# Optimization experiments

Measured on AMD Instinct MI355X. Metric: run time of the kernel, lower is better.

Reference implementation:

```python
import jax, jax.numpy as jnp
import numpy as np

N_NODES = 100000
N_EDGES = 1000000
D_FEAT = 128
N_ACTIONS = 64


def setup_inputs() -> dict:
    key = jax.random.key(0)
    ks = jax.random.split(key, 8)
    return {
        "x": jax.random.normal(ks[0], (N_NODES, D_FEAT), dtype=jnp.float32),
        "edge_index": jax.random.randint(ks[1], (2, N_EDGES), 0, N_NODES, dtype=jnp.int64),
        "W_gcn": jax.random.normal(ks[2], (D_FEAT, D_FEAT), dtype=jnp.float32) / np.sqrt(D_FEAT),
        "b_gcn": jax.random.normal(ks[3], (D_FEAT,), dtype=jnp.float32) * 0.02,
        "W_high": jax.random.normal(ks[4], (D_FEAT, N_ACTIONS), dtype=jnp.float32) / np.sqrt(D_FEAT),
        "b_high": jax.random.normal(ks[5], (N_ACTIONS,), dtype=jnp.float32) * 0.02,
        "W_low": jax.random.normal(ks[6], (D_FEAT, N_ACTIONS), dtype=jnp.float32) / np.sqrt(D_FEAT),
        "b_low": jax.random.normal(ks[7], (N_ACTIONS,), dtype=jnp.float32) * 0.02,
    }


def gcn_conv(x, edge_index, W, b):
    """PyG GCNConv: add self-loops, symmetric normalization, aggregate, linear."""
    n = x.shape[0]
    loops = jnp.arange(n, dtype=edge_index.dtype)
    src = jnp.concatenate([edge_index[0], loops])  # message sources
    dst = jnp.concatenate([edge_index[1], loops])  # message targets
    # degree of each target node (edge weight 1, incl. self-loop)
    deg = jax.ops.segment_sum(jnp.ones(src.shape[0], dtype=x.dtype), dst, num_segments=n)
    dinv = jax.lax.rsqrt(deg)  # deg >= 1 thanks to self-loops
    norm = dinv[src] * dinv[dst]  # [E+N]
    h = x @ W  # [N, D] dense transform first (cheaper than transforming messages)
    agg = jax.ops.segment_sum(h[src] * norm[:, None], dst, num_segments=n)
    return agg + b


def reference(x, edge_index, W_gcn, b_gcn, W_high, b_high, W_low, b_low):
    h = gcn_conv(x, edge_index, W_gcn, b_gcn)  # [N, D]
    high = h @ W_high + b_high  # [N, A]
    low = h @ W_low + b_low     # [N, A]
    return (high, low)
```

## Files before the change

### kernel.cpp

```cpp
#include <hip/hip_runtime.h>


#define BLOCK 256
#define SB 512
#define NB_MAX 784
#define CONV_BLOCKS 4096

typedef _Float16 half8 __attribute__((ext_vector_type(8)));
typedef _Float16 half2v __attribute__((ext_vector_type(2)));
typedef float f32x4 __attribute__((ext_vector_type(4)));

__device__ inline unsigned short f2bf(float f) {
    unsigned u = __float_as_uint(f);
    unsigned r = (u + 0x7FFF + ((u >> 16) & 1)) >> 16;
    return (unsigned short)r;
}
__device__ inline float bf2f(unsigned short u) {
    return __uint_as_float(((unsigned)u) << 16);
}


__global__ __launch_bounds__(BLOCK) void k_prep(const float* __restrict__ x,
                                                const int* __restrict__ dst, int E,
                                                const float* __restrict__ Wg,
                                                const float* __restrict__ Wh,
                                                const float* __restrict__ Wl,
                                                const float* __restrict__ bg,
                                                const float* __restrict__ bh,
                                                const float* __restrict__ bl,
                                                _Float16* __restrict__ WfT,
                                                float* __restrict__ bf,
                                                int* __restrict__ hist_g,
                                                unsigned short* __restrict__ xh,
                                                int n, int NB) {
    __shared__ int hist[NB_MAX];
    int b = blockIdx.x;
    if (b < 16) {
        int r = b * 8 + (threadIdx.x >> 5);
        int c0 = (threadIdx.x & 31) * 4;
        float a0 = 0.f, a1 = 0.f, a2 = 0.f, a3 = 0.f;
        for (int j = 0; j < 128; j++) {
            float wg = Wg[r * 128 + j];
            float4 wc;
            if (c0 < 64) wc = *(const float4*)(Wh + j * 64 + c0);
            else         wc = *(const float4*)(Wl + j * 64 + (c0 - 64));
            a0 += wg * wc.x; a1 += wg * wc.y; a2 += wg * wc.z; a3 += wg * wc.w;
        }
        WfT[(size_t)(c0 + 0) * 128 + r] = (_Float16)a0;
        WfT[(size_t)(c0 + 1) * 128 + r] = (_Float16)a1;
        WfT[(size_t)(c0 + 2) * 128 + r] = (_Float16)a2;
        WfT[(size_t)(c0 + 3) * 128 + r] = (_Float16)a3;
    } else if (b == 16) {
        int c = threadIdx.x;
        if (c < 128) {
            float acc = (c < 64) ? bh[c] : bl[c - 64];
            for (int j = 0; j < 128; j++) {
                float wc = (c < 64) ? Wh[j * 64 + c] : Wl[j * 64 + (c - 64)];
                acc += bg[j] * wc;
            }
            bf[c] = acc;
        }
    } else if (b < 17 + SB) {
        int blk = b - 17;
        for (int i = threadIdx.x; i < NB; i += BLOCK) hist[i] = 0;
        __syncthreads();
        int chunk = (E + SB - 1) / SB;
        int e0 = blk * chunk, e1 = min(E, e0 + chunk);
        for (int e = e0 + threadIdx.x; e < e1; e += BLOCK)
            atomicAdd(&hist[dst[e] >> 7], 1);
        __syncthreads();
        for (int i = threadIdx.x; i < NB; i += BLOCK)
            hist_g[(size_t)i * SB + blk] = hist[i];
    } else {
        const float4* x4 = (const float4*)x;
        ushort4* o4 = (ushort4*)xh;
        int total = n * 32;
        int i = (b - 17 - SB) * BLOCK + threadIdx.x;
        int stride = CONV_BLOCKS * BLOCK;
        for (; i < total; i += stride) {
            float4 v = x4[i];
            ushort4 o;
            o.x = f2bf(v.x); o.y = f2bf(v.y); o.z = f2bf(v.z); o.w = f2bf(v.w);
            o4[i] = o;
        }
    }
}


__global__ __launch_bounds__(BLOCK) void k_scanA(int* __restrict__ hist_g,
                                                 int* __restrict__ bucketTotal, int NB) {
    __shared__ int s[SB];
    int bkt = blockIdx.x;
    int t = threadIdx.x;
    int a0 = hist_g[(size_t)bkt * SB + t];
    int a1 = hist_g[(size_t)bkt * SB + t + 256];
    s[t] = a0; s[t + 256] = a1;
    __syncthreads();
    for (int ofs = 1; ofs < SB; ofs <<= 1) {
        int v0 = (t >= ofs) ? s[t - ofs] : 0;
        int v1 = (t + 256 >= ofs) ? s[t + 256 - ofs] : 0;
        __syncthreads();
        s[t] += v0; s[t + 256] += v1;
        __syncthreads();
    }
    hist_g[(size_t)bkt * SB + t] = s[t] - a0;
    hist_g[(size_t)bkt * SB + t + 256] = s[t + 256] - a1;
    if (t == 255) bucketTotal[bkt] = s[SB - 1];
}


__global__ __launch_bounds__(1024) void k_scanB(const int* __restrict__ bucketTotal,
                                                int* __restrict__ bucketStart,
                                                int NB, int E) {
    __shared__ int s[1024];
    int t = threadIdx.x;
    int v = (t < NB) ? bucketTotal[t] : 0;
    s[t] = v;
    __syncthreads();
    for (int ofs = 1; ofs < 1024; ofs <<= 1) {
        int u = (t >= ofs) ? s[t - ofs] : 0;
        __syncthreads();
        s[t] += u;
        __syncthreads();
    }
    if (t < NB) bucketStart[t] = s[t] - v;
    if (t == NB - 1) bucketStart[NB] = E;
}


__global__ __launch_bounds__(BLOCK) void k_scatter(const int* __restrict__ src,
                                                   const int* __restrict__ dst, int E,
                                                   const int* __restrict__ hist_g,
                                                   const int* __restrict__ bucketStart,
                                                   int2* __restrict__ ebuf, int NB) {
    __shared__ int cur[NB_MAX];
    int blk = blockIdx.x;
    for (int i = threadIdx.x; i < NB; i += BLOCK)
        cur[i] = bucketStart[i] + hist_g[(size_t)i * SB + blk];
    __syncthreads();
    int chunk = (E + SB - 1) / SB;
    int e0 = blk * chunk, e1 = min(E, e0 + chunk);
    for (int e = e0 + threadIdx.x; e < e1; e += BLOCK) {
        int d = dst[e];
        int pos = atomicAdd(&cur[d >> 7], 1);
        ebuf[pos] = make_int2(d, src[e]);
    }
}


__global__ __launch_bounds__(BLOCK) void k_node(const int2* __restrict__ ebuf,
                                                const int* __restrict__ bucketStart,
                                                int* __restrict__ off,
                                                float* __restrict__ dinv,
                                                int* __restrict__ csr,
                                                int n, int NB, int E) {
    __shared__ int cnt[128];
    __shared__ int pre[128];
    __shared__ int cur[128];
    int bkt = blockIdx.x;
    int t = threadIdx.x;
    int node0 = bkt << 7;
    int nn = min(128, n - node0);
    int eb0 = bucketStart[bkt], eb1 = bucketStart[bkt + 1];

    if (t < 128) cnt[t] = 0;
    __syncthreads();
    for (int e = eb0 + t; e < eb1; e += BLOCK)
        atomicAdd(&cnt[ebuf[e].x & 127], 1);
    __syncthreads();
    if (t < 128) pre[t] = cnt[t];
    __syncthreads();
    for (int ofs = 1; ofs < 128; ofs <<= 1) {
        int v = (t < 128 && t >= ofs) ? pre[t - ofs] : 0;
        __syncthreads();
        if (t < 128) pre[t] += v;
        __syncthreads();
    }
    if (t < 128) cur[t] = pre[t] - cnt[t];
    __syncthreads();
    if (t < nn) {
        off[node0 + t] = eb0 + cur[t];
        dinv[node0 + t] = rsqrtf((float)(cnt[t] + 1));
    }
    if (bkt == 0 && t == 0) off[n] = E;
    for (int e = eb0 + t; e < eb1; e += BLOCK) {
        int2 p = ebuf[e];
        int pos = atomicAdd(&cur[p.x & 127], 1);
        csr[eb0 + pos] = p.y;
    }
}


__global__ __launch_bounds__(BLOCK) void k_gather(const int* __restrict__ off,
                                                  const int* __restrict__ csr,
                                                  const float* __restrict__ dinv,
                                                  const unsigned short* __restrict__ xh,
                                                  const float* __restrict__ x,
                                                  _Float16* __restrict__ aggh, int n) {
    int wave = (blockIdx.x * blockDim.x + threadIdx.x) >> 6;
    int lane = threadIdx.x & 63;
    if (wave >= n) return;
    int d = wave;
    int beg = off[d], end = off[d + 1];

    float accx = 0.f, accy = 0.f;
    for (int base = beg; base < end; base += 64) {
        int cnt = min(64, end - base);
        int s = 0; float w = 0.f;
        if (lane < cnt) { s = csr[base + lane]; w = dinv[s]; }
        int j = 0;
        for (; j + 4 <= cnt; j += 4) {
            int s0 = __shfl(s, j);
            int s1 = __shfl(s, j + 1);
            int s2 = __shfl(s, j + 2);
            int s3 = __shfl(s, j + 3);
            float w0 = __shfl(w, j);
            float w1 = __shfl(w, j + 1);
            float w2 = __shfl(w, j + 2);
            float w3 = __shfl(w, j + 3);
            ushort2 v0 = ((const ushort2*)(xh + (size_t)s0 * 128))[lane];
            ushort2 v1 = ((const ushort2*)(xh + (size_t)s1 * 128))[lane];
            ushort2 v2 = ((const ushort2*)(xh + (size_t)s2 * 128))[lane];
            ushort2 v3 = ((const ushort2*)(xh + (size_t)s3 * 128))[lane];
            accx += w0 * bf2f(v0.x) + w1 * bf2f(v1.x) + w2 * bf2f(v2.x) + w3 * bf2f(v3.x);
            accy += w0 * bf2f(v0.y) + w1 * bf2f(v1.y) + w2 * bf2f(v2.y) + w3 * bf2f(v3.y);
        }
        for (; j < cnt; j++) {
            int sj = __shfl(s, j);
            float wj = __shfl(w, j);
            ushort2 v = ((const ushort2*)(xh + (size_t)sj * 128))[lane];
            accx += wj * bf2f(v.x);
            accy += wj * bf2f(v.y);
        }
    }
    float dv = dinv[d];
    float2 xv = ((const float2*)(x + (size_t)d * 128))[lane];
    half2v o;
    o.x = (_Float16)(dv * accx + dv * dv * xv.x);
    o.y = (_Float16)(dv * accy + dv * dv * xv.y);
    ((half2v*)(aggh + (size_t)d * 128))[lane] = o;
}


__global__ __launch_bounds__(BLOCK) void k_final(const _Float16* __restrict__ aggh,
                                                 const _Float16* __restrict__ WfT,
                                                 const float* __restrict__ bf,
                                                 float* __restrict__ out, int n) {
    int wave = threadIdx.x >> 6;
    int lane = threadIdx.x & 63;
    int l15 = lane & 15;
    int lk = lane >> 4;
    int row_base = blockIdx.x * 128 + wave * 32;

    half8 a[2][4];
#pragma unroll
    for (int rf = 0; rf < 2; rf++) {
        int r = row_base + rf * 16 + l15;
        if (r >= n) r = n - 1;
        const _Float16* ap = aggh + (size_t)r * 128 + lk * 8;
#pragma unroll
        for (int kk = 0; kk < 4; kk++)
            a[rf][kk] = *(const half8*)(ap + kk * 32);
    }

    f32x4 acc[2][8];
#pragma unroll
    for (int rf = 0; rf < 2; rf++)
#pragma unroll
        for (int cf = 0; cf < 8; cf++)
            acc[rf][cf] = (f32x4){0.f, 0.f, 0.f, 0.f};

#pragma unroll
    for (int kk = 0; kk < 4; kk++) {
#pragma unroll
        for (int cf = 0; cf < 8; cf++) {
            const _Float16* bp = WfT + (size_t)(cf * 16 + l15) * 128 + kk * 32 + lk * 8;
            half8 bfr = *(const half8*)bp;
#pragma unroll
            for (int rf = 0; rf < 2; rf++)
                acc[rf][cf] = __builtin_amdgcn_mfma_f32_16x16x32_f16(
                    a[rf][kk], bfr, acc[rf][cf], 0, 0, 0);
        }
    }

#pragma unroll
    for (int cf = 0; cf < 8; cf++) {
        int c = cf * 16 + l15;
        float bv = bf[c];
        size_t cbase = (c < 64) ? (size_t)c : (size_t)n * 64 + (size_t)(c - 64);
#pragma unroll
        for (int rf = 0; rf < 2; rf++) {
            int r0 = row_base + rf * 16 + lk * 4;
#pragma unroll
            for (int j = 0; j < 4; j++) {
                int r = r0 + j;
                if (r < n) out[cbase + (size_t)r * 64] = acc[rf][cf][j] + bv;
            }
        }
    }
}

extern "C" void kernel_launch(void* const* d_in, const int* in_sizes, int n_in,
                              void* d_out, int out_size, void* d_ws, size_t ws_size,
                              hipStream_t stream) {
    const float* x  = (const float*)d_in[0];
    const int*   ei = (const int*)d_in[1];
    const float* Wg = (const float*)d_in[2];
    const float* bg = (const float*)d_in[3];
    const float* Wh = (const float*)d_in[4];
    const float* bh = (const float*)d_in[5];
    const float* Wl = (const float*)d_in[6];
    const float* bl = (const float*)d_in[7];
    float* out = (float*)d_out;

    int n = in_sizes[0] / 128;
    int E = in_sizes[1] / 2;
    const int* src = ei;
    const int* dst = ei + E;
    int NB = (n + 127) >> 7;

    char* ws = (char*)d_ws;
    int*   hist_g      = (int*)ws;                ws += (size_t)NB_MAX * SB * 4;
    int*   bucketTotal = (int*)ws;                ws += (size_t)NB_MAX * 4;
    int*   bucketStart = (int*)ws;                ws += (size_t)(NB_MAX + 2) * 4;
    int2*  ebuf        = (int2*)ws;               ws += (size_t)E * 8;
    int*   off         = (int*)ws;                ws += (size_t)(n + 1) * 4;
    float* dinv        = (float*)ws;              ws += (size_t)n * 4;
    int*   csr         = (int*)ws;                ws += (size_t)E * 4;
    _Float16* aggh     = (_Float16*)ws;           ws += (size_t)n * 128 * 2;
    _Float16* WfT      = (_Float16*)ws;           ws += (size_t)128 * 128 * 2;
    float* bf          = (float*)ws;              ws += (size_t)128 * 4;
    unsigned short* xh = (unsigned short*)ws;

    k_prep<<<17 + SB + CONV_BLOCKS, BLOCK, 0, stream>>>(
        x, dst, E, Wg, Wh, Wl, bg, bh, bl, WfT, bf, hist_g, xh, n, NB);
    k_scanA<<<NB, BLOCK, 0, stream>>>(hist_g, bucketTotal, NB);
    k_scanB<<<1, 1024, 0, stream>>>(bucketTotal, bucketStart, NB, E);
    k_scatter<<<SB, BLOCK, 0, stream>>>(src, dst, E, hist_g, bucketStart, ebuf, NB);
    k_node<<<NB, BLOCK, 0, stream>>>(ebuf, bucketStart, off, dinv, csr, n, NB, E);
    k_gather<<<((size_t)n * 64 + BLOCK - 1) / BLOCK, BLOCK, 0, stream>>>(
        off, csr, dinv, xh, x, aggh, n);
    k_final<<<(n + 127) / 128, BLOCK, 0, stream>>>(aggh, WfT, bf, out, n);
}
```

Measured before the change: 273.2 us.

## Gather with 16-byte half8 loads, four edges per wave step, fp16 features

The gather kernel now splits each wave into four 16-lane groups. Each group processes a different edge and each lane loads 16 bytes (8 fp16 values), where before the whole wave walked one edge with 4-byte loads. Partial sums are combined across groups with xor shuffles, and the self-loop term now reads the fp16 copy instead of the fp32 input. The staged features switch from bf16 to fp16, and workspace buffers get 256-byte alignment. The wider loads and more edges in flight are meant to raise memory-level parallelism. The cost is extra reduction shuffles, wasted lanes when an edge chunk is not a multiple of four (handled via zero weights), and fp16 range and precision tradeoffs.

```diff
diff --git a/kernel.cpp b/kernel.cpp
--- a/kernel.cpp
+++ b/kernel.cpp
@@ -7,17 +7,8 @@
 #define CONV_BLOCKS 4096
 
 typedef _Float16 half8 __attribute__((ext_vector_type(8)));
-typedef _Float16 half2v __attribute__((ext_vector_type(2)));
+typedef _Float16 half4 __attribute__((ext_vector_type(4)));
 typedef float f32x4 __attribute__((ext_vector_type(4)));
-
-__device__ inline unsigned short f2bf(float f) {
-    unsigned u = __float_as_uint(f);
-    unsigned r = (u + 0x7FFF + ((u >> 16) & 1)) >> 16;
-    return (unsigned short)r;
-}
-__device__ inline float bf2f(unsigned short u) {
-    return __uint_as_float(((unsigned)u) << 16);
-}
 
 
 __global__ __launch_bounds__(BLOCK) void k_prep(const float* __restrict__ x,
@@ -31,7 +22,7 @@
                                                 _Float16* __restrict__ WfT,
                                                 float* __restrict__ bf,
                                                 int* __restrict__ hist_g,
-                                                unsigned short* __restrict__ xh,
+                                                _Float16* __restrict__ xh,
                                                 int n, int NB) {
     __shared__ int hist[NB_MAX];
     int b = blockIdx.x;
@@ -73,14 +64,15 @@
             hist_g[(size_t)i * SB + blk] = hist[i];
     } else {
         const float4* x4 = (const float4*)x;
-        ushort4* o4 = (ushort4*)xh;
+        half4* o4 = (half4*)xh;
         int total = n * 32;
         int i = (b - 17 - SB) * BLOCK + threadIdx.x;
         int stride = CONV_BLOCKS * BLOCK;
         for (; i < total; i += stride) {
             float4 v = x4[i];
-            ushort4 o;
-            o.x = f2bf(v.x); o.y = f2bf(v.y); o.z = f2bf(v.z); o.w = f2bf(v.w);
+            half4 o;
+            o.x = (_Float16)v.x; o.y = (_Float16)v.y;
+            o.z = (_Float16)v.z; o.w = (_Float16)v.w;
             o4[i] = o;
         }
     }
@@ -194,51 +186,49 @@
 __global__ __launch_bounds__(BLOCK) void k_gather(const int* __restrict__ off,
                                                   const int* __restrict__ csr,
                                                   const float* __restrict__ dinv,
-                                                  const unsigned short* __restrict__ xh,
-                                                  const float* __restrict__ x,
+                                                  const _Float16* __restrict__ xh,
                                                   _Float16* __restrict__ aggh, int n) {
     int wave = (blockIdx.x * blockDim.x + threadIdx.x) >> 6;
     int lane = threadIdx.x & 63;
     if (wave >= n) return;
     int d = wave;
     int beg = off[d], end = off[d + 1];
-
-    float accx = 0.f, accy = 0.f;
+    int g = lane >> 4;
+    int sl = lane & 15;
+
+    float acc[8];
+#pragma unroll
+    for (int k = 0; k < 8; k++) acc[k] = 0.f;
+
     for (int base = beg; base < end; base += 64) {
         int cnt = min(64, end - base);
         int s = 0; float w = 0.f;
         if (lane < cnt) { s = csr[base + lane]; w = dinv[s]; }
-        int j = 0;
-        for (; j + 4 <= cnt; j += 4) {
-            int s0 = __shfl(s, j);
-            int s1 = __shfl(s, j + 1);
-            int s2 = __shfl(s, j + 2);
-            int s3 = __shfl(s, j + 3);
-            float w0 = __shfl(w, j);
-            float w1 = __shfl(w, j + 1);
-            float w2 = __shfl(w, j + 2);
-            float w3 = __shfl(w, j + 3);
-            ushort2 v0 = ((const ushort2*)(xh + (size_t)s0 * 128))[lane];
-            ushort2 v1 = ((const ushort2*)(xh + (size_t)s1 * 128))[lane];
-            ushort2 v2 = ((const ushort2*)(xh + (size_t)s2 * 128))[lane];
-            ushort2 v3 = ((const ushort2*)(xh + (size_t)s3 * 128))[lane];
-            accx += w0 * bf2f(v0.x) + w1 * bf2f(v1.x) + w2 * bf2f(v2.x) + w3 * bf2f(v3.x);
-            accy += w0 * bf2f(v0.y) + w1 * bf2f(v1.y) + w2 * bf2f(v2.y) + w3 * bf2f(v3.y);
-        }
-        for (; j < cnt; j++) {
-            int sj = __shfl(s, j);
-            float wj = __shfl(w, j);
-            ushort2 v = ((const ushort2*)(xh + (size_t)sj * 128))[lane];
-            accx += wj * bf2f(v.x);
-            accy += wj * bf2f(v.y);
-        }
-    }
+        for (int j = 0; j < cnt; j += 4) {
+            int e = j + g;
+            int se = __shfl(s, e);
+            float we = __shfl(w, e);
+            half8 v = *(const half8*)(xh + (size_t)se * 128 + sl * 8);
+#pragma unroll
+            for (int k = 0; k < 8; k++)
+                acc[k] += we * (float)v[k];
+        }
+    }
+
+#pragma unroll
+    for (int k = 0; k < 8; k++) {
+        acc[k] += __shfl_xor(acc[k], 16);
+        acc[k] += __shfl_xor(acc[k], 32);
+    }
+
     float dv = dinv[d];
-    float2 xv = ((const float2*)(x + (size_t)d * 128))[lane];
-    half2v o;
-    o.x = (_Float16)(dv * accx + dv * dv * xv.x);
-    o.y = (_Float16)(dv * accy + dv * dv * xv.y);
-    ((half2v*)(aggh + (size_t)d * 128))[lane] = o;
+    half8 xv = *(const half8*)(xh + (size_t)d * 128 + sl * 8);
+    half8 o;
+#pragma unroll
+    for (int k = 0; k < 8; k++)
+        o[k] = (_Float16)(dv * (acc[k] + dv * (float)xv[k]));
+    if (lane < 16)
+        *(half8*)(aggh + (size_t)d * 128 + sl * 8) = o;
 }
 
 
@@ -319,18 +309,23 @@
     const int* dst = ei + E;
     int NB = (n + 127) >> 7;
 
-    char* ws = (char*)d_ws;
-    int*   hist_g      = (int*)ws;                ws += (size_t)NB_MAX * SB * 4;
-    int*   bucketTotal = (int*)ws;                ws += (size_t)NB_MAX * 4;
-    int*   bucketStart = (int*)ws;                ws += (size_t)(NB_MAX + 2) * 4;
-    int2*  ebuf        = (int2*)ws;               ws += (size_t)E * 8;
-    int*   off         = (int*)ws;                ws += (size_t)(n + 1) * 4;
-    float* dinv        = (float*)ws;              ws += (size_t)n * 4;
-    int*   csr         = (int*)ws;                ws += (size_t)E * 4;
-    _Float16* aggh     = (_Float16*)ws;           ws += (size_t)n * 128 * 2;
-    _Float16* WfT      = (_Float16*)ws;           ws += (size_t)128 * 128 * 2;
-    float* bf          = (float*)ws;              ws += (size_t)128 * 4;
-    unsigned short* xh = (unsigned short*)ws;
+#define WS_TAKE(ptr, type, count)                                        \
+    ptr = (type*)wsp;                                                    \
+    wsp = (char*)(((size_t)(wsp + (size_t)(count) * sizeof(type)) + 255) \
+                  & ~(size_t)255)
+
+    char* wsp = (char*)d_ws;
+    int*      hist_g;      WS_TAKE(hist_g,      int,      (size_t)NB_MAX * SB);
+    int*      bucketTotal; WS_TAKE(bucketTotal, int,      NB_MAX);
+    int*      bucketStart; WS_TAKE(bucketStart, int,      NB_MAX + 1);
+    int2*     ebuf;        WS_TAKE(ebuf,        int2,     E);
+    int*      off;         WS_TAKE(off,         int,      n + 1);
+    float*    dinv;        WS_TAKE(dinv,        float,    n);
+    int*      csr;         WS_TAKE(csr,         int,      E);
+    _Float16* aggh;        WS_TAKE(aggh,        _Float16, (size_t)n * 128);
+    _Float16* WfT;         WS_TAKE(WfT,         _Float16, 128 * 128);
+    float*    bf;          WS_TAKE(bf,          float,    128);
+    _Float16* xh;          WS_TAKE(xh,          _Float16, (size_t)n * 128);
 
     k_prep<<<17 + SB + CONV_BLOCKS, BLOCK, 0, stream>>>(
         x, dst, E, Wg, Wh, Wl, bg, bh, bl, WfT, bf, hist_g, xh, n, NB);
@@ -339,6 +334,6 @@
     k_scatter<<<SB, BLOCK, 0, stream>>>(src, dst, E, hist_g, bucketStart, ebuf, NB);
     k_node<<<NB, BLOCK, 0, stream>>>(ebuf, bucketStart, off, dinv, csr, n, NB, E);
     k_gather<<<((size_t)n * 64 + BLOCK - 1) / BLOCK, BLOCK, 0, stream>>>(
-        off, csr, dinv, xh, x, aggh, n);
+        off, csr, dinv, xh, aggh, n);
     k_final<<<(n + 127) / 128, BLOCK, 0, stream>>>(aggh, WfT, bf, out, n);
 }
```

Result: faster. 259.4 us (-5.1%).
